# Kernel tuning notes

Measured on AMD Instinct MI355X. Metric: run time of the kernel, lower is better.

The kernel has to match this reference:

```python
import jax, jax.numpy as jnp
import numpy as np

D_MODEL = 768
N_LAYER = 2
VOCAB = 32000
D_STATE = 16
D_INNER = 1536
DT_RANK = 48
D_CONV = 4
B, L = 2, 1024
EPS = 1e-5


def rmsnorm(x, w):
    return x * jax.lax.rsqrt(jnp.mean(x * x, axis=-1, keepdims=True) + EPS) * w


def selective_scan(u, dt, A, Bm, Cm, Dv):
    # u: (b,l,d)  dt: (b,l,d)  A: (d,n)  Bm,Cm: (b,l,n)  Dv: (d,)
    dA = jnp.einsum('bld,dn->bldn', dt, A)
    dB_u = jnp.einsum('bld,bld,bln->bldn', dt, u, Bm)
    # shift dA left by one step along l, zero-pad at end, reverse-cumsum, exp
    t = jnp.concatenate([dA[:, 1:], jnp.zeros_like(dA[:, :1])], axis=1)
    dA_cumsum = jnp.exp(jnp.flip(jnp.cumsum(jnp.flip(t, axis=1), axis=1), axis=1))
    x = dB_u * dA_cumsum
    x = jnp.cumsum(x, axis=1) / (dA_cumsum + 1e-12)
    y = jnp.einsum('bldn,bln->bld', x, Cm)
    return y + u * Dv


def mamba_block(x, W_in, conv_w, conv_b, x_proj_w, dt_proj_w, dt_proj_b, A_log, D_param, W_out):
    b, l, d = x.shape
    xz = x @ W_in.T                       # (b,l,2*d_inner)
    xs, res = xz[..., :D_INNER], xz[..., D_INNER:]
    # depthwise causal conv1d: left-pad d_conv-1 -> output length l
    xt = jnp.transpose(xs, (0, 2, 1))     # (b,d_in,l)
    xt = jax.lax.conv_general_dilated(
        xt, conv_w, window_strides=(1,), padding=[(D_CONV - 1, 0)],
        dimension_numbers=('NCH', 'OIH', 'NCH'), feature_group_count=D_INNER)
    xt = xt + conv_b[None, :, None]
    xs = jax.nn.silu(jnp.transpose(xt, (0, 2, 1)))
    # SSM
    A = -jnp.exp(A_log.astype(jnp.float32))
    x_dbl = xs @ x_proj_w.T               # (b,l,dt_rank+2n)
    delta = x_dbl[..., :DT_RANK]
    Bm = x_dbl[..., DT_RANK:DT_RANK + D_STATE]
    Cm = x_dbl[..., DT_RANK + D_STATE:]
    delta = jax.nn.softplus(delta @ dt_proj_w.T + dt_proj_b)
    y = selective_scan(xs, delta, A, Bm, Cm, D_param.astype(jnp.float32))
    y = y * jax.nn.silu(res)
    return y @ W_out.T


def setup_inputs() -> dict:
    key = jax.random.key(0)
    ks = jax.random.split(key, 12)
    s = 0.02
    inp = {
        'input_ids': jax.random.randint(ks[0], (B, L), 0, VOCAB),
        'embedding': jax.random.normal(ks[1], (VOCAB, D_MODEL), jnp.float32) * s,
        'W_in': jax.random.normal(ks[2], (N_LAYER, 2 * D_INNER, D_MODEL), jnp.float32) * s,
        'conv_w': jax.random.normal(ks[3], (N_LAYER, D_INNER, 1, D_CONV), jnp.float32) * 0.2,
        'conv_b': jnp.zeros((N_LAYER, D_INNER), jnp.float32),
        'x_proj_w': jax.random.normal(ks[4], (N_LAYER, DT_RANK + 2 * D_STATE, D_INNER), jnp.float32) * s,
        'dt_proj_w': jax.random.normal(ks[5], (N_LAYER, D_INNER, DT_RANK), jnp.float32) * s,
        'dt_proj_b': jnp.full((N_LAYER, D_INNER), -4.0, jnp.float32),
        'A_log': jnp.broadcast_to(jnp.log(jnp.arange(1, D_STATE + 1, dtype=jnp.float32)), (N_LAYER, D_INNER, D_STATE)) * jnp.ones((N_LAYER, D_INNER, 1), jnp.float32),
        'D_param': jnp.ones((N_LAYER, D_INNER), jnp.float32),
        'W_out': jax.random.normal(ks[6], (N_LAYER, D_MODEL, D_INNER), jnp.float32) * s,
        'norm_w': jnp.ones((N_LAYER, D_MODEL), jnp.float32),
        'norm_f_w': jnp.ones((D_MODEL,), jnp.float32),
    }
    return inp


def reference(input_ids, embedding, W_in, conv_w, conv_b, x_proj_w, dt_proj_w,
              dt_proj_b, A_log, D_param, W_out, norm_w, norm_f_w):
    x = embedding[input_ids]              # (b,l,d_model)
    for i in range(N_LAYER):
        x = mamba_block(rmsnorm(x, norm_w[i]), W_in[i], conv_w[i], conv_b[i],
                        x_proj_w[i], dt_proj_w[i], dt_proj_b[i], A_log[i],
                        D_param[i], W_out[i]) + x
    x = rmsnorm(x, norm_f_w)
    return x @ embedding.T                # tied lm_head -> (b,l,vocab)
```

## Files before the change

### kernel.cpp

```cpp
#include <hip/hip_runtime.h>
#include <math.h>

#define DM    768
#define DS    16
#define DI    1536
#define DTR   48
#define NB    2
#define NL    1024
#define NBL   (NB*NL)
#define NVOC  32000
#define XDL   128

typedef __attribute__((ext_vector_type(8))) short bf16x8;
typedef __attribute__((ext_vector_type(4))) float floatx4;

static __device__ __forceinline__ float siluf(float x){ return x / (1.0f + expf(-x)); }
static __device__ __forceinline__ float softplusf(float x){ return (x > 20.0f) ? x : log1pf(expf(x)); }
static __device__ __forceinline__ unsigned short f2bf(float f){
    unsigned int u = __float_as_uint(f);
    u += 0x7FFFu + ((u >> 16) & 1u);
    return (unsigned short)(u >> 16);
}

#define GLL16(g, l) __builtin_amdgcn_global_load_lds( \
    (const __attribute__((address_space(1))) unsigned int*)(g), \
    (__attribute__((address_space(3))) unsigned int*)(l), 16, 0, 0)

__global__ __launch_bounds__(256) void cast_bf16_kernel(const float* __restrict__ in,
        unsigned short* __restrict__ out, int n4){
    int i = blockIdx.x*256 + threadIdx.x;
    if (i >= n4) return;
    float4 v = ((const float4*)in)[i];
    ushort4 o = { f2bf(v.x), f2bf(v.y), f2bf(v.z), f2bf(v.w) };
    ((ushort4*)out)[i] = o;
}

__global__ __launch_bounds__(256) void cast_pad_xproj_kernel(const float* __restrict__ in,
        unsigned short* __restrict__ out){
    int q = blockIdx.x*256 + threadIdx.x;
    const int QL = 128*1536/4;
    if (q >= 2*QL) return;
    int layer = q / QL, rem = q - layer*QL;
    int row = rem / (1536/4), c4 = rem - row*(1536/4);
    ushort4 o = {0,0,0,0};
    if (row < 80){
        float4 v = ((const float4*)(in + ((size_t)layer*80 + row)*1536))[c4];
        o.x = f2bf(v.x); o.y = f2bf(v.y); o.z = f2bf(v.z); o.w = f2bf(v.w);
    }
    ((ushort4*)out)[q] = o;
}

__global__ __launch_bounds__(256) void zero_f32_kernel(float* __restrict__ p, int n4){
    int i = blockIdx.x*256 + threadIdx.x;
    if (i >= n4) return;
    float4 z = {0.f,0.f,0.f,0.f};
    ((float4*)p)[i] = z;
}

__global__ __launch_bounds__(256) void embed_kernel(const int* __restrict__ ids,
        const float* __restrict__ emb, float* __restrict__ x){
    int i = blockIdx.x*256 + threadIdx.x;
    if (i >= NBL*DM) return;
    int row = i / DM, c = i - row*DM;
    x[i] = emb[(size_t)ids[row]*DM + c];
}

__global__ __launch_bounds__(256) void rmsnorm_bf16_kernel(const float* __restrict__ x,
        const float* __restrict__ w, unsigned short* __restrict__ h){
    int row = blockIdx.x;
    const float* xr = x + (size_t)row*DM;
    __shared__ float red[4];
    int tid = threadIdx.x, lane = tid & 63, wv = tid >> 6;
    float s = 0.f;
    for (int c = tid; c < DM; c += 256){ float v = xr[c]; s += v*v; }
    #pragma unroll
    for (int o = 32; o > 0; o >>= 1) s += __shfl_xor(s, o, 64);
    if (lane == 0) red[wv] = s;
    __syncthreads();
    float tot = red[0] + red[1] + red[2] + red[3];
    float r = 1.0f / sqrtf(tot*(1.0f/DM) + 1e-5f);
    for (int c = tid; c < DM; c += 256) h[(size_t)row*DM + c] = f2bf(xr[c]*r*w[c]);
}

template<int MODE>
__global__ __launch_bounds__(256) void mfma_gemm_nt(const unsigned short* __restrict__ A,
        const unsigned short* __restrict__ B, float* __restrict__ C,
        int M, int N, int K, int Kc){
    __shared__ __align__(16) unsigned short Asm[2][128*64];
    __shared__ __align__(16) unsigned short Bsm[2][128*64];
    int tid = threadIdx.x;

    int nwg  = gridDim.x * gridDim.y;
    int orig = blockIdx.y * gridDim.x + blockIdx.x;
    int q = nwg >> 3, r = nwg & 7;
    int xcd = orig & 7;
    int wg  = (xcd < r ? xcd*(q+1) : r*(q+1) + (xcd-r)*q) + (orig >> 3);
    int mb  = wg % gridDim.y;
    int nb  = wg / gridDim.y;
    int m0 = mb * 128, n0 = nb * 128;

    int lane = tid & 63;
    int quad = lane >> 4, l16 = lane & 15;
    int wave = tid >> 6;
    int wm = (wave >> 1) * 64, wn = (wave & 1) * 64;

    floatx4 acc[4][4] = {};

    int srow = tid >> 3;
    int csrc = ((tid & 7) ^ ((tid >> 3) & 7)) * 8;
    const unsigned short* Ag = A + (size_t)(m0 + srow) * K + csrc;
    const unsigned short* Bg = B + (size_t)(n0 + srow) * K + csrc;

    int k0 = blockIdx.z * Kc;
    int nsteps = Kc >> 6;

    #pragma unroll
    for (int qr = 0; qr < 4; qr++){
        GLL16(Ag + (size_t)qr*32*K + k0, &Asm[0][(qr*256 + tid)*8]);
        GLL16(Bg + (size_t)qr*32*K + k0, &Bsm[0][(qr*256 + tid)*8]);
    }
    __syncthreads();

    int cur = 0;
    for (int s = 0; s < nsteps; s++){
        if (s + 1 < nsteps){
            int kt = k0 + (s+1)*64;
            #pragma unroll
            for (int qr = 0; qr < 4; qr++){
                GLL16(Ag + (size_t)qr*32*K + kt, &Asm[cur^1][(qr*256 + tid)*8]);
                GLL16(Bg + (size_t)qr*32*K + kt, &Bsm[cur^1][(qr*256 + tid)*8]);
            }
        }

        #pragma unroll
        for (int ks = 0; ks < 2; ks++){
            bf16x8 af[4], bff[4];
            #pragma unroll
            for (int i = 0; i < 4; i++){
                int ar = wm + i*16 + l16;
                af[i]  = *(const bf16x8*)&Asm[cur][ar*64 + ((ks*4 + quad) ^ (ar & 7))*8];
                int br = wn + i*16 + l16;
                bff[i] = *(const bf16x8*)&Bsm[cur][br*64 + ((ks*4 + quad) ^ (br & 7))*8];
            }
            #pragma unroll
            for (int i = 0; i < 4; i++)
                #pragma unroll
                for (int j = 0; j < 4; j++)
                    acc[i][j] = __builtin_amdgcn_mfma_f32_16x16x32_bf16(af[i], bff[j], acc[i][j], 0, 0, 0);
        }
        __syncthreads();
        cur ^= 1;
    }

    #pragma unroll
    for (int i = 0; i < 4; i++){
        int gm = m0 + wm + i*16 + quad*4;
        #pragma unroll
        for (int j = 0; j < 4; j++){
            int gn = n0 + wn + j*16 + l16;
            float* cp = C + (size_t)gm*N + gn;
            #pragma unroll
            for (int rr = 0; rr < 4; rr++){
                float v = acc[i][j][rr];
                if (MODE == 2){
                    atomicAdd(&cp[(size_t)rr*N], v);
                } else {
                    if (MODE == 1) v += cp[(size_t)rr*N];
                    cp[(size_t)rr*N] = v;
                }
            }
        }
    }
}

__global__ __launch_bounds__(256) void gemm_nt(const float* __restrict__ A,
        const float* __restrict__ Bw, float* __restrict__ C, const float* __restrict__ bias,
        int M, int N, int K, int lda, int ldb, int ldc, int act, int accum){
    __shared__ float As[16][68];
    __shared__ float Bs[16][68];
    int tid = threadIdx.x;
    int tn = tid & 15, tm = tid >> 4;
    int n0 = blockIdx.x * 64, m0 = blockIdx.y * 64;
    float acc[4][4] = {{0.f}};
    for (int kt = 0; kt < K; kt += 16){
        int gk = kt + tn;
        bool kok = gk < K;
        #pragma unroll
        for (int r = 0; r < 4; r++){
            int m = tm + r*16;
            As[tn][m] = (kok && (m0 + m) < M) ? A[(size_t)(m0+m)*lda + gk] : 0.f;
            Bs[tn][m] = (kok && (n0 + m) < N) ? Bw[(size_t)(n0+m)*ldb + gk] : 0.f;
        }
        __syncthreads();
        #pragma unroll
        for (int kk = 0; kk < 16; kk++){
            float a0 = As[kk][tm*4+0], a1 = As[kk][tm*4+1], a2 = As[kk][tm*4+2], a3 = As[kk][tm*4+3];
            float b0 = Bs[kk][tn*4+0], b1 = Bs[kk][tn*4+1], b2 = Bs[kk][tn*4+2], b3 = Bs[kk][tn*4+3];
            acc[0][0] += a0*b0; acc[0][1] += a0*b1; acc[0][2] += a0*b2; acc[0][3] += a0*b3;
            acc[1][0] += a1*b0; acc[1][1] += a1*b1; acc[1][2] += a1*b2; acc[1][3] += a1*b3;
            acc[2][0] += a2*b0; acc[2][1] += a2*b1; acc[2][2] += a2*b2; acc[2][3] += a2*b3;
            acc[3][0] += a3*b0; acc[3][1] += a3*b1; acc[3][2] += a3*b2; acc[3][3] += a3*b3;
        }
        __syncthreads();
    }
    #pragma unroll
    for (int i = 0; i < 4; i++){
        int gm = m0 + tm*4 + i;
        if (gm >= M) continue;
        #pragma unroll
        for (int j = 0; j < 4; j++){
            int gn = n0 + tn*4 + j;
            if (gn >= N) continue;
            float v = acc[i][j];
            if (bias) v += bias[gn];
            if (act == 1) v = softplusf(v);
            size_t ci = (size_t)gm*ldc + gn;
            if (accum) v += C[ci];
            C[ci] = v;
        }
    }
}

__global__ __launch_bounds__(256) void conv_silu_kernel(const float* __restrict__ xz,
        const float* __restrict__ cw, const float* __restrict__ cb,
        float* __restrict__ xs, unsigned short* __restrict__ xs_bf){
    int i = blockIdx.x*256 + threadIdx.x;
    if (i >= NBL*DI) return;
    int bl = i / DI, d = i - bl*DI;
    int l = bl & (NL-1);
    float acc = cb[d];
    #pragma unroll
    for (int j = 0; j < 4; j++){
        int off = j - 3;
        if (l + off >= 0) acc += cw[d*4+j] * xz[(size_t)(bl + off)*(2*DI) + d];
    }
    float v = siluf(acc);
    xs[i] = v;
    xs_bf[i] = f2bf(v);
}

__global__ __launch_bounds__(256) void transpose_kernel(const float* __restrict__ in,
        float* __restrict__ out, int R, int Ccols, int ldin){
    __shared__ float tile[32][33];
    int c0 = blockIdx.x*32, r0 = blockIdx.y*32;
    int tx = threadIdx.x & 31, ty = threadIdx.x >> 5;
    #pragma unroll
    for (int i = 0; i < 32; i += 8){
        int r = r0 + ty + i, c = c0 + tx;
        tile[ty+i][tx] = (r < R && c < Ccols) ? in[(size_t)r*ldin + c] : 0.f;
    }
    __syncthreads();
    #pragma unroll
    for (int i = 0; i < 32; i += 8){
        int r = r0 + tx, c = c0 + ty + i;
        if (c < Ccols && r < R) out[(size_t)c*R + r] = tile[tx][ty+i];
    }
}

__global__ __launch_bounds__(256) void transpose2_kernel(const float* __restrict__ in1,
        float* __restrict__ out1, const float* __restrict__ in2, float* __restrict__ out2){
    __shared__ float tile[32][33];
    int c0 = blockIdx.x*32, r0 = blockIdx.y*32;
    int tx = threadIdx.x & 31, ty = threadIdx.x >> 5;
    #pragma unroll
    for (int i = 0; i < 32; i += 8)
        tile[ty+i][tx] = in1[(size_t)(r0+ty+i)*DI + (c0+tx)];
    __syncthreads();
    #pragma unroll
    for (int i = 0; i < 32; i += 8)
        out1[(size_t)(c0+ty+i)*NBL + (r0+tx)] = tile[tx][ty+i];
    __syncthreads();
    #pragma unroll
    for (int i = 0; i < 32; i += 8)
        tile[ty+i][tx] = in2[(size_t)(r0+ty+i)*DI + (c0+tx)];
    __syncthreads();
    #pragma unroll
    for (int i = 0; i < 32; i += 8)
        out2[(size_t)(c0+ty+i)*NBL + (r0+tx)] = tile[tx][ty+i];
}

static __device__ __forceinline__ float wave_incl_scan(float v, int lane){
    #pragma unroll
    for (int s = 1; s < 64; s <<= 1){
        float t = __shfl_up(v, s, 64);
        if (lane >= s) v += t;
    }
    return v;
}

__global__ __launch_bounds__(256) void scan_kernel(const float* __restrict__ u_t,
        const float* dt_t, const float* __restrict__ xdbl_t,
        const float* __restrict__ A_log, const float* __restrict__ Dp,
        float* y_t){
    int tid = threadIdx.x, lane = tid & 63, w = tid >> 6;
    int bd = blockIdx.x*4 + w;
    int b = bd / DI, d = bd - b*DI;
    size_t rowoff = (size_t)d*NBL + b*NL;
    int l0 = lane*16;

    float d16[16], u16[16];
    #pragma unroll
    for (int q = 0; q < 4; q++){
        float4 v = ((const float4*)(dt_t + rowoff + l0))[q];
        d16[q*4+0]=v.x; d16[q*4+1]=v.y; d16[q*4+2]=v.z; d16[q*4+3]=v.w;
        float4 u = ((const float4*)(u_t + rowoff + l0))[q];
        u16[q*4+0]=u.x; u16[q*4+1]=u.y; u16[q*4+2]=u.z; u16[q*4+3]=u.w;
    }
    float pl[16], yac[16];
    float run = 0.f;
    #pragma unroll
    for (int r = 0; r < 16; r++){ run += d16[r]; pl[r] = run; yac[r] = 0.f; }
    float inc = wave_incl_scan(run, lane);
    float ex  = inc - run;
    float T   = __shfl(inc, 63, 64);
    #pragma unroll
    for (int r = 0; r < 16; r++) pl[r] += ex;

    for (int n = 0; n < DS; n++){
        float An = -expf(A_log[d*DS + n]);
        float Bv[16], Cv[16];
        #pragma unroll
        for (int q = 0; q < 4; q++){
            float4 bv = ((const float4*)(xdbl_t + (size_t)(DTR+n)*NBL + b*NL + l0))[q];
            Bv[q*4+0]=bv.x; Bv[q*4+1]=bv.y; Bv[q*4+2]=bv.z; Bv[q*4+3]=bv.w;
            float4 cv = ((const float4*)(xdbl_t + (size_t)(DTR+DS+n)*NBL + b*NL + l0))[q];
            Cv[q*4+0]=cv.x; Cv[q*4+1]=cv.y; Cv[q*4+2]=cv.z; Cv[q*4+3]=cv.w;
        }
        float e[16], zl[16];
        float zrun = 0.f;
        #pragma unroll
        for (int r = 0; r < 16; r++){
            e[r] = expf(An * (T - pl[r]));
            zrun += d16[r]*u16[r]*Bv[r]*e[r];
            zl[r] = zrun;
        }
        float zinc = wave_incl_scan(zrun, lane);
        float zex  = zinc - zrun;
        #pragma unroll
        for (int r = 0; r < 16; r++){
            float num = zex + zl[r];
            yac[r] += num / (e[r] + 1e-12f) * Cv[r];
        }
    }
    float Dv = Dp[d];
    #pragma unroll
    for (int q = 0; q < 4; q++){
        float4 yo;
        yo.x = yac[q*4+0] + u16[q*4+0]*Dv;
        yo.y = yac[q*4+1] + u16[q*4+1]*Dv;
        yo.z = yac[q*4+2] + u16[q*4+2]*Dv;
        yo.w = yac[q*4+3] + u16[q*4+3]*Dv;
        ((float4*)(y_t + rowoff + l0))[q] = yo;
    }
}

__global__ __launch_bounds__(256) void gate_transpose_kernel(const float* __restrict__ y_t,
        const float* __restrict__ xz, unsigned short* __restrict__ ys){
    __shared__ float tile[32][33];
    int c0 = blockIdx.x*32;
    int r0 = blockIdx.y*32;
    int tx = threadIdx.x & 31, ty = threadIdx.x >> 5;
    #pragma unroll
    for (int i = 0; i < 32; i += 8)
        tile[ty+i][tx] = y_t[(size_t)(r0+ty+i)*NBL + (c0+tx)];
    __syncthreads();
    #pragma unroll
    for (int i = 0; i < 32; i += 8){
        int d  = r0 + tx;
        int bl = c0 + ty + i;
        float g = siluf(xz[(size_t)bl*(2*DI) + DI + d]);
        ys[(size_t)bl*DI + d] = f2bf(tile[tx][ty+i] * g);
    }
}

extern "C" void kernel_launch(void* const* d_in, const int* in_sizes, int n_in,
                              void* d_out, int out_size, void* d_ws, size_t ws_size,
                              hipStream_t stream){
    const int*   ids    = (const int*)d_in[0];
    const float* emb    = (const float*)d_in[1];
    const float* W_in   = (const float*)d_in[2];
    const float* convw  = (const float*)d_in[3];
    const float* convb  = (const float*)d_in[4];
    const float* xproj  = (const float*)d_in[5];
    const float* dtw    = (const float*)d_in[6];
    const float* dtbias = (const float*)d_in[7];
    const float* Alog   = (const float*)d_in[8];
    const float* Dpar   = (const float*)d_in[9];
    const float* Wout   = (const float*)d_in[10];
    const float* normw  = (const float*)d_in[11];
    const float* normf  = (const float*)d_in[12];
    float* out = (float*)d_out;

    float* ws    = (float*)d_ws;
    float* x     = ws;
    float* xz    = x     + (size_t)NBL*DM;
    float* xs    = xz    + (size_t)NBL*2*DI;
    float* xdbl  = xs    + (size_t)NBL*DI;
    float* xdblt = xdbl  + (size_t)NBL*XDL;
    float* dtb   = xdblt + (size_t)NBL*80;
    float* dtt   = dtb   + (size_t)NBL*DI;
    float* ut    = dtt   + (size_t)NBL*DI;
    unsigned short* h_bf   = (unsigned short*)(ut + (size_t)NBL*DI);
    unsigned short* emb_bf = h_bf    + (size_t)NBL*DM;
    unsigned short* win_bf = emb_bf  + (size_t)NVOC*DM;
    unsigned short* wout_bf= win_bf  + (size_t)2*2*DI*DM;
    unsigned short* xs_bf  = wout_bf + (size_t)2*DM*DI;
    unsigned short* xprojp = xs_bf   + (size_t)NBL*DI;
    unsigned short* ys_bf  = (unsigned short*)dtb;
    float* yt = dtt;

    cast_bf16_kernel<<<(NVOC*DM/4 + 255)/256, 256, 0, stream>>>(emb, emb_bf, NVOC*DM/4);
    cast_bf16_kernel<<<(2*2*DI*DM/4 + 255)/256, 256, 0, stream>>>(W_in, win_bf, 2*2*DI*DM/4);
    cast_bf16_kernel<<<(2*DM*DI/4 + 255)/256, 256, 0, stream>>>(Wout, wout_bf, 2*DM*DI/4);
    cast_pad_xproj_kernel<<<(2*128*1536/4 + 255)/256, 256, 0, stream>>>(xproj, xprojp);

    embed_kernel<<<(NBL*DM + 255)/256, 256, 0, stream>>>(ids, emb, x);

    for (int i = 0; i < 2; i++){
        rmsnorm_bf16_kernel<<<NBL, 256, 0, stream>>>(x, normw + i*DM, h_bf);
        mfma_gemm_nt<0><<<dim3(3072/128, NBL/128, 1), 256, 0, stream>>>(
                h_bf, win_bf + (size_t)i*2*DI*DM, xz, NBL, 2*DI, DM, DM);
        conv_silu_kernel<<<(NBL*DI + 255)/256, 256, 0, stream>>>(xz, convw + i*DI*4, convb + i*DI, xs, xs_bf);
        zero_f32_kernel<<<(NBL*XDL/4 + 255)/256, 256, 0, stream>>>(xdbl, NBL*XDL/4);
        mfma_gemm_nt<2><<<dim3(1, NBL/128, 8), 256, 0, stream>>>(
                xs_bf, xprojp + (size_t)i*128*DI, xdbl, NBL, XDL, DI, DI/8);
        gemm_nt<<<dim3(24,32), 256, 0, stream>>>(xdbl, dtw + (size_t)i*DI*DTR, dtb, dtbias + i*DI,
                NBL, DI, DTR, XDL, DTR, DI, 1, 0);
        transpose_kernel<<<dim3(3,64),  256, 0, stream>>>(xdbl, xdblt, NBL, 80, XDL);
        transpose2_kernel<<<dim3(48,64), 256, 0, stream>>>(dtb, dtt, xs, ut);
        scan_kernel<<<NB*DI/4, 256, 0, stream>>>(ut, dtt, xdblt,
                Alog + (size_t)i*DI*DS, Dpar + i*DI, yt);
        gate_transpose_kernel<<<dim3(64,48), 256, 0, stream>>>(yt, xz, ys_bf);
        mfma_gemm_nt<2><<<dim3(DM/128, NBL/128, 2), 256, 0, stream>>>(
                ys_bf, wout_bf + (size_t)i*DM*DI, x, NBL, DM, DI, DI/2);
    }

    rmsnorm_bf16_kernel<<<NBL, 256, 0, stream>>>(x, normf, h_bf);
    mfma_gemm_nt<0><<<dim3(NVOC/128, NBL/128, 1), 256, 0, stream>>>(
            h_bf, emb_bf, out, NBL, NVOC, DM, DM);
}
```

Baseline: 877.6 us.

## Triple-buffer MFMA GEMM with BK=32 and move dt_proj onto MFMA with fused softplus

The shared bf16 MFMA GEMM moves from a double-buffered K-step of 64 to a triple-buffered K-step of 32. It uses explicit vmcnt waits and a single barrier per step, so global-to-LDS loads run two stages ahead of compute. Separately, the scalar fp32 dt_proj GEMM is replaced by the MFMA GEMM with a new epilogue mode that adds the bias and applies softplus. That path needs an extra cast of x_dbl to bf16 and a zero-padded bf16 copy of dt_proj_w, and it adds bf16 rounding to delta.

```diff
diff --git a/kernel.cpp b/kernel.cpp
--- a/kernel.cpp
+++ b/kernel.cpp
@@ -50,6 +50,19 @@
     ((ushort4*)out)[q] = o;
 }
 
+__global__ __launch_bounds__(256) void cast_pad_dtw_kernel(const float* __restrict__ in,
+        unsigned short* __restrict__ out){
+    int q = blockIdx.x*256 + threadIdx.x;
+    if (q >= 2*1536*32) return;
+    int row = q >> 5, qc = q & 31;
+    ushort4 o = {0,0,0,0};
+    if (qc < 12){
+        float4 v = *(const float4*)(in + (size_t)row*48 + qc*4);
+        o.x = f2bf(v.x); o.y = f2bf(v.y); o.z = f2bf(v.z); o.w = f2bf(v.w);
+    }
+    ((ushort4*)out)[q] = o;
+}
+
 __global__ __launch_bounds__(256) void zero_f32_kernel(float* __restrict__ p, int n4){
     int i = blockIdx.x*256 + threadIdx.x;
     if (i >= n4) return;
@@ -85,9 +98,9 @@
 template<int MODE>
 __global__ __launch_bounds__(256) void mfma_gemm_nt(const unsigned short* __restrict__ A,
         const unsigned short* __restrict__ B, float* __restrict__ C,
-        int M, int N, int K, int Kc){
-    __shared__ __align__(16) unsigned short Asm[2][128*64];
-    __shared__ __align__(16) unsigned short Bsm[2][128*64];
+        const float* __restrict__ bias, int M, int N, int K, int Kc){
+    __shared__ __align__(16) unsigned short Asm[3][128*32];
+    __shared__ __align__(16) unsigned short Bsm[3][128*32];
     int tid = threadIdx.x;
 
     int nwg  = gridDim.x * gridDim.y;
@@ -106,51 +119,60 @@
 
     floatx4 acc[4][4] = {};
 
-    int srow = tid >> 3;
-    int csrc = ((tid & 7) ^ ((tid >> 3) & 7)) * 8;
+    int srow = tid >> 2;
+    int csrc = ((tid & 3) ^ ((tid >> 2) & 3) ^ ((tid >> 4) & 3)) * 8;
     const unsigned short* Ag = A + (size_t)(m0 + srow) * K + csrc;
     const unsigned short* Bg = B + (size_t)(n0 + srow) * K + csrc;
+    size_t half = (size_t)64 * K;
 
     int k0 = blockIdx.z * Kc;
-    int nsteps = Kc >> 6;
-
-    #pragma unroll
-    for (int qr = 0; qr < 4; qr++){
-        GLL16(Ag + (size_t)qr*32*K + k0, &Asm[0][(qr*256 + tid)*8]);
-        GLL16(Bg + (size_t)qr*32*K + k0, &Bsm[0][(qr*256 + tid)*8]);
-    }
-    __syncthreads();
+    int nsteps = Kc >> 5;
+
+#define STAGE(buf, step) do{ int kk_ = k0 + (step)*32;                      \
+        GLL16(Ag + kk_,        &Asm[buf][(size_t)tid*8]);                   \
+        GLL16(Ag + kk_ + half, &Asm[buf][2048 + (size_t)tid*8]);            \
+        GLL16(Bg + kk_,        &Bsm[buf][(size_t)tid*8]);                   \
+        GLL16(Bg + kk_ + half, &Bsm[buf][2048 + (size_t)tid*8]); }while(0)
+#define WAITV4 asm volatile("s_waitcnt vmcnt(4)" ::: "memory")
+#define WAITV0 asm volatile("s_waitcnt vmcnt(0)" ::: "memory")
+
+    STAGE(0, 0);
+    if (nsteps > 1) STAGE(1, 1);
+    if (nsteps > 1) { WAITV4; } else { WAITV0; }
+    __builtin_amdgcn_s_barrier();
+    __builtin_amdgcn_sched_barrier(0);
 
     int cur = 0;
     for (int s = 0; s < nsteps; s++){
+        if (s + 2 < nsteps){
+            int b2 = cur + 2; if (b2 >= 3) b2 -= 3;
+            STAGE(b2, s + 2);
+        }
+
+        bf16x8 af[4], bff[4];
+        #pragma unroll
+        for (int i = 0; i < 4; i++){
+            int ar = wm + i*16 + l16;
+            af[i]  = *(const bf16x8*)&Asm[cur][ar*32 + ((quad ^ (ar & 3) ^ ((ar >> 2) & 3)))*8];
+            int br = wn + i*16 + l16;
+            bff[i] = *(const bf16x8*)&Bsm[cur][br*32 + ((quad ^ (br & 3) ^ ((br >> 2) & 3)))*8];
+        }
+        #pragma unroll
+        for (int i = 0; i < 4; i++)
+            #pragma unroll
+            for (int j = 0; j < 4; j++)
+                acc[i][j] = __builtin_amdgcn_mfma_f32_16x16x32_bf16(af[i], bff[j], acc[i][j], 0, 0, 0);
+
         if (s + 1 < nsteps){
-            int kt = k0 + (s+1)*64;
-            #pragma unroll
-            for (int qr = 0; qr < 4; qr++){
-                GLL16(Ag + (size_t)qr*32*K + kt, &Asm[cur^1][(qr*256 + tid)*8]);
-                GLL16(Bg + (size_t)qr*32*K + kt, &Bsm[cur^1][(qr*256 + tid)*8]);
-            }
-        }
-
-        #pragma unroll
-        for (int ks = 0; ks < 2; ks++){
-            bf16x8 af[4], bff[4];
-            #pragma unroll
-            for (int i = 0; i < 4; i++){
-                int ar = wm + i*16 + l16;
-                af[i]  = *(const bf16x8*)&Asm[cur][ar*64 + ((ks*4 + quad) ^ (ar & 7))*8];
-                int br = wn + i*16 + l16;
-                bff[i] = *(const bf16x8*)&Bsm[cur][br*64 + ((ks*4 + quad) ^ (br & 7))*8];
-            }
-            #pragma unroll
-            for (int i = 0; i < 4; i++)
-                #pragma unroll
-                for (int j = 0; j < 4; j++)
-                    acc[i][j] = __builtin_amdgcn_mfma_f32_16x16x32_bf16(af[i], bff[j], acc[i][j], 0, 0, 0);
-        }
-        __syncthreads();
-        cur ^= 1;
-    }
+            if (s + 2 < nsteps) { WAITV4; } else { WAITV0; }
+            __builtin_amdgcn_s_barrier();
+            __builtin_amdgcn_sched_barrier(0);
+            cur = (cur + 1 == 3) ? 0 : cur + 1;
+        }
+    }
+#undef STAGE
+#undef WAITV4
+#undef WAITV0
 
     #pragma unroll
     for (int i = 0; i < 4; i++){
@@ -164,59 +186,13 @@
                 float v = acc[i][j][rr];
                 if (MODE == 2){
                     atomicAdd(&cp[(size_t)rr*N], v);
+                } else if (MODE == 3){
+                    cp[(size_t)rr*N] = softplusf(v + bias[gn]);
                 } else {
                     if (MODE == 1) v += cp[(size_t)rr*N];
                     cp[(size_t)rr*N] = v;
                 }
             }
-        }
-    }
-}
-
-__global__ __launch_bounds__(256) void gemm_nt(const float* __restrict__ A,
-        const float* __restrict__ Bw, float* __restrict__ C, const float* __restrict__ bias,
-        int M, int N, int K, int lda, int ldb, int ldc, int act, int accum){
-    __shared__ float As[16][68];
-    __shared__ float Bs[16][68];
-    int tid = threadIdx.x;
-    int tn = tid & 15, tm = tid >> 4;
-    int n0 = blockIdx.x * 64, m0 = blockIdx.y * 64;
-    float acc[4][4] = {{0.f}};
-    for (int kt = 0; kt < K; kt += 16){
-        int gk = kt + tn;
-        bool kok = gk < K;
-        #pragma unroll
-        for (int r = 0; r < 4; r++){
-            int m = tm + r*16;
-            As[tn][m] = (kok && (m0 + m) < M) ? A[(size_t)(m0+m)*lda + gk] : 0.f;
-            Bs[tn][m] = (kok && (n0 + m) < N) ? Bw[(size_t)(n0+m)*ldb + gk] : 0.f;
-        }
-        __syncthreads();
-        #pragma unroll
-        for (int kk = 0; kk < 16; kk++){
-            float a0 = As[kk][tm*4+0], a1 = As[kk][tm*4+1], a2 = As[kk][tm*4+2], a3 = As[kk][tm*4+3];
-            float b0 = Bs[kk][tn*4+0], b1 = Bs[kk][tn*4+1], b2 = Bs[kk][tn*4+2], b3 = Bs[kk][tn*4+3];
-            acc[0][0] += a0*b0; acc[0][1] += a0*b1; acc[0][2] += a0*b2; acc[0][3] += a0*b3;
-            acc[1][0] += a1*b0; acc[1][1] += a1*b1; acc[1][2] += a1*b2; acc[1][3] += a1*b3;
-            acc[2][0] += a2*b0; acc[2][1] += a2*b1; acc[2][2] += a2*b2; acc[2][3] += a2*b3;
-            acc[3][0] += a3*b0; acc[3][1] += a3*b1; acc[3][2] += a3*b2; acc[3][3] += a3*b3;
-        }
-        __syncthreads();
-    }
-    #pragma unroll
-    for (int i = 0; i < 4; i++){
-        int gm = m0 + tm*4 + i;
-        if (gm >= M) continue;
-        #pragma unroll
-        for (int j = 0; j < 4; j++){
-            int gn = n0 + tn*4 + j;
-            if (gn >= N) continue;
-            float v = acc[i][j];
-            if (bias) v += bias[gn];
-            if (act == 1) v = softplusf(v);
-            size_t ci = (size_t)gm*ldc + gn;
-            if (accum) v += C[ci];
-            C[ci] = v;
         }
     }
 }
@@ -406,6 +382,8 @@
     unsigned short* wout_bf= win_bf  + (size_t)2*2*DI*DM;
     unsigned short* xs_bf  = wout_bf + (size_t)2*DM*DI;
     unsigned short* xprojp = xs_bf   + (size_t)NBL*DI;
+    unsigned short* xdbl_bf= xprojp  + (size_t)2*128*DI;
+    unsigned short* dtw_bf = xdbl_bf + (size_t)NBL*XDL;
     unsigned short* ys_bf  = (unsigned short*)dtb;
     float* yt = dtt;
 
@@ -413,29 +391,31 @@
     cast_bf16_kernel<<<(2*2*DI*DM/4 + 255)/256, 256, 0, stream>>>(W_in, win_bf, 2*2*DI*DM/4);
     cast_bf16_kernel<<<(2*DM*DI/4 + 255)/256, 256, 0, stream>>>(Wout, wout_bf, 2*DM*DI/4);
     cast_pad_xproj_kernel<<<(2*128*1536/4 + 255)/256, 256, 0, stream>>>(xproj, xprojp);
+    cast_pad_dtw_kernel<<<(2*1536*32 + 255)/256, 256, 0, stream>>>(dtw, dtw_bf);
 
     embed_kernel<<<(NBL*DM + 255)/256, 256, 0, stream>>>(ids, emb, x);
 
     for (int i = 0; i < 2; i++){
         rmsnorm_bf16_kernel<<<NBL, 256, 0, stream>>>(x, normw + i*DM, h_bf);
         mfma_gemm_nt<0><<<dim3(3072/128, NBL/128, 1), 256, 0, stream>>>(
-                h_bf, win_bf + (size_t)i*2*DI*DM, xz, NBL, 2*DI, DM, DM);
+                h_bf, win_bf + (size_t)i*2*DI*DM, xz, nullptr, NBL, 2*DI, DM, DM);
         conv_silu_kernel<<<(NBL*DI + 255)/256, 256, 0, stream>>>(xz, convw + i*DI*4, convb + i*DI, xs, xs_bf);
         zero_f32_kernel<<<(NBL*XDL/4 + 255)/256, 256, 0, stream>>>(xdbl, NBL*XDL/4);
         mfma_gemm_nt<2><<<dim3(1, NBL/128, 8), 256, 0, stream>>>(
-                xs_bf, xprojp + (size_t)i*128*DI, xdbl, NBL, XDL, DI, DI/8);
-        gemm_nt<<<dim3(24,32), 256, 0, stream>>>(xdbl, dtw + (size_t)i*DI*DTR, dtb, dtbias + i*DI,
-                NBL, DI, DTR, XDL, DTR, DI, 1, 0);
+                xs_bf, xprojp + (size_t)i*128*DI, xdbl, nullptr, NBL, XDL, DI, DI/8);
+        cast_bf16_kernel<<<(NBL*XDL/4 + 255)/256, 256, 0, stream>>>(xdbl, xdbl_bf, NBL*XDL/4);
+        mfma_gemm_nt<3><<<dim3(DI/128, NBL/128, 1), 256, 0, stream>>>(
+                xdbl_bf, dtw_bf + (size_t)i*DI*XDL, dtb, dtbias + i*DI, NBL, DI, XDL, XDL);
         transpose_kernel<<<dim3(3,64),  256, 0, stream>>>(xdbl, xdblt, NBL, 80, XDL);
         transpose2_kernel<<<dim3(48,64), 256, 0, stream>>>(dtb, dtt, xs, ut);
         scan_kernel<<<NB*DI/4, 256, 0, stream>>>(ut, dtt, xdblt,
                 Alog + (size_t)i*DI*DS, Dpar + i*DI, yt);
         gate_transpose_kernel<<<dim3(64,48), 256, 0, stream>>>(yt, xz, ys_bf);
         mfma_gemm_nt<2><<<dim3(DM/128, NBL/128, 2), 256, 0, stream>>>(
-                ys_bf, wout_bf + (size_t)i*DM*DI, x, NBL, DM, DI, DI/2);
+                ys_bf, wout_bf + (size_t)i*DM*DI, x, nullptr, NBL, DM, DI, DI/2);
     }
 
     rmsnorm_bf16_kernel<<<NBL, 256, 0, stream>>>(x, normf, h_bf);
     mfma_gemm_nt<0><<<dim3(NVOC/128, NBL/128, 1), 256, 0, stream>>>(
-            h_bf, emb_bf, out, NBL, NVOC, DM, DM);
-}
+            h_bf, emb_bf, out, nullptr, NBL, NVOC, DM, DM);
+}
```

Result: no change. 886.7 us (+1.0%).

## Add 256x256 ping-pong GEMM for LM head and triple-buffer generic MFMA GEMM

Applied to the files above, without the earlier changes.

Adds a new 512-thread GEMM with 256x256 tiles for the vocab projection. It interleaves global-to-LDS loads with MFMA phases using explicit vmcnt waits, barriers and priority hints, so memory traffic overlaps with compute. The existing 128x128 GEMM moves to K=32 steps with a three-stage LDS buffer, a new swizzle, and waitcnt-based synchronisation in place of __syncthreads. An unused bias parameter is added. The risk lies in the hand-tuned waitcnt counts, which must match the load order exactly, and in higher register and LDS pressure.

```diff
diff --git a/kernel.cpp b/kernel.cpp
--- a/kernel.cpp
+++ b/kernel.cpp
@@ -25,6 +25,9 @@
 #define GLL16(g, l) __builtin_amdgcn_global_load_lds( \
     (const __attribute__((address_space(1))) unsigned int*)(g), \
     (__attribute__((address_space(3))) unsigned int*)(l), 16, 0, 0)
+
+#define WAITVM(n) do{ asm volatile("s_waitcnt vmcnt(" #n ")" ::: "memory"); \
+                      __builtin_amdgcn_sched_barrier(0); }while(0)
 
 __global__ __launch_bounds__(256) void cast_bf16_kernel(const float* __restrict__ in,
         unsigned short* __restrict__ out, int n4){
@@ -82,12 +85,158 @@
     for (int c = tid; c < DM; c += 256) h[(size_t)row*DM + c] = f2bf(xr[c]*r*w[c]);
 }
 
+__global__ __launch_bounds__(512, 2) void gemm256(const unsigned short* __restrict__ A,
+        const unsigned short* __restrict__ B, float* __restrict__ C,
+        int M, int N, int K){
+    __shared__ __align__(16) unsigned short Asm[2][2][128*64];
+    __shared__ __align__(16) unsigned short Bsm[2][2][128*64];
+    int tid = threadIdx.x;
+
+    int nwg  = gridDim.x * gridDim.y;
+    int orig = blockIdx.y * gridDim.x + blockIdx.x;
+    int qq = nwg >> 3, r8 = nwg & 7;
+    int xcd = orig & 7;
+    int wg  = (xcd < r8 ? xcd*(qq+1) : r8*(qq+1) + (xcd-r8)*qq) + (orig >> 3);
+    int mb  = wg % gridDim.y;
+    int nb  = wg / gridDim.y;
+    int m0 = mb*256, n0 = nb*256;
+
+    int lane = tid & 63, wave = tid >> 6;
+    int wr = wave >> 2, wc = wave & 3;
+    int quad = lane >> 4, l16 = lane & 15;
+
+    int srow = tid >> 3;
+    int csrc = ((tid & 7) ^ ((tid >> 3) & 7)) * 8;
+    const unsigned short* Ag = A + (size_t)(m0 + srow)*K + csrc;
+    const unsigned short* Bg = B + (size_t)(n0 + srow)*K + csrc;
+    int NT = K >> 6;
+
+    floatx4 acc[8][4] = {};
+
+#define ST_A(tt, h) do{ \
+    GLL16(Ag + (size_t)((h)*128)*K      + (size_t)(tt)*64, &Asm[(tt)&1][h][(size_t)tid*8]); \
+    GLL16(Ag + (size_t)((h)*128 + 64)*K + (size_t)(tt)*64, &Asm[(tt)&1][h][4096 + (size_t)tid*8]); \
+}while(0)
+#define ST_B(tt, h) do{ \
+    GLL16(Bg + (size_t)((h)*128)*K      + (size_t)(tt)*64, &Bsm[(tt)&1][h][(size_t)tid*8]); \
+    GLL16(Bg + (size_t)((h)*128 + 64)*K + (size_t)(tt)*64, &Bsm[(tt)&1][h][4096 + (size_t)tid*8]); \
+}while(0)
+#define LDA_(tt, h, jj, ks) (*(const bf16x8*)&Asm[(tt)&1][h][((jj)*32 + wr*16 + l16)*64 + ((((ks)*4 + quad) ^ (l16 & 7))*8)])
+#define LDB_(tt, k, ks)     (*(const bf16x8*)&Bsm[(tt)&1][wc>>1][((wc&1)*64 + (k)*16 + l16)*64 + ((((ks)*4 + quad) ^ (l16 & 7))*8)])
+#define MM(d, x, y) d = __builtin_amdgcn_mfma_f32_16x16x32_bf16(x, y, d, 0, 0, 0)
+
+    ST_A(0, 0); ST_B(0, 0); ST_B(0, 1); ST_A(0, 1);
+    if (NT > 1){ ST_A(1, 0); ST_B(1, 0); ST_B(1, 1); WAITVM(8); }
+    else       { WAITVM(0); }
+    __builtin_amdgcn_s_barrier();
+
+    for (int t = 0; t < NT; ++t){
+        bf16x8 a[8], b0[4], b1[4];
+        #pragma unroll
+        for (int jj = 0; jj < 4; jj++){
+            a[jj*2+0] = LDA_(t, 0, jj, 0);
+            a[jj*2+1] = LDA_(t, 0, jj, 1);
+        }
+        #pragma unroll
+        for (int k = 0; k < 2; k++){
+            b0[k*2+0] = LDB_(t, k, 0);
+            b0[k*2+1] = LDB_(t, k, 1);
+        }
+        if (t + 1 < NT) ST_A(t+1, 1);
+        __builtin_amdgcn_s_barrier();
+        __builtin_amdgcn_s_setprio(1);
+        #pragma unroll
+        for (int jj = 0; jj < 4; jj++)
+            #pragma unroll
+            for (int fn = 0; fn < 2; fn++){
+                MM(acc[jj][fn], a[jj*2+0], b0[fn*2+0]);
+                MM(acc[jj][fn], a[jj*2+1], b0[fn*2+1]);
+            }
+        __builtin_amdgcn_s_setprio(0);
+        __builtin_amdgcn_s_barrier();
+
+        #pragma unroll
+        for (int k = 0; k < 2; k++){
+            b1[k*2+0] = LDB_(t, k+2, 0);
+            b1[k*2+1] = LDB_(t, k+2, 1);
+        }
+        if (t + 2 < NT) ST_A(t+2, 0);
+        __builtin_amdgcn_s_barrier();
+        __builtin_amdgcn_s_setprio(1);
+        #pragma unroll
+        for (int jj = 0; jj < 4; jj++)
+            #pragma unroll
+            for (int fn = 0; fn < 2; fn++){
+                MM(acc[jj][fn+2], a[jj*2+0], b1[fn*2+0]);
+                MM(acc[jj][fn+2], a[jj*2+1], b1[fn*2+1]);
+            }
+        __builtin_amdgcn_s_setprio(0);
+        if (t == NT-1)      { WAITVM(0); }
+        else if (t == NT-2) { WAITVM(8); }
+        else                { WAITVM(10); }
+        __builtin_amdgcn_s_barrier();
+
+        #pragma unroll
+        for (int jj = 0; jj < 4; jj++){
+            a[jj*2+0] = LDA_(t, 1, jj, 0);
+            a[jj*2+1] = LDA_(t, 1, jj, 1);
+        }
+        if (t + 2 < NT) ST_B(t+2, 0);
+        __builtin_amdgcn_s_barrier();
+        __builtin_amdgcn_s_setprio(1);
+        #pragma unroll
+        for (int jj = 0; jj < 4; jj++)
+            #pragma unroll
+            for (int fn = 0; fn < 2; fn++){
+                MM(acc[4+jj][fn], a[jj*2+0], b0[fn*2+0]);
+                MM(acc[4+jj][fn], a[jj*2+1], b0[fn*2+1]);
+            }
+        __builtin_amdgcn_s_setprio(0);
+        __builtin_amdgcn_s_barrier();
+
+        if (t + 2 < NT) ST_B(t+2, 1);
+        __builtin_amdgcn_s_barrier();
+        __builtin_amdgcn_s_setprio(1);
+        #pragma unroll
+        for (int jj = 0; jj < 4; jj++)
+            #pragma unroll
+            for (int fn = 0; fn < 2; fn++){
+                MM(acc[4+jj][fn+2], a[jj*2+0], b1[fn*2+0]);
+                MM(acc[4+jj][fn+2], a[jj*2+1], b1[fn*2+1]);
+            }
+        __builtin_amdgcn_s_setprio(0);
+        if (t + 1 < NT){
+            if (t == NT-2) { WAITVM(2); }
+            else           { WAITVM(8); }
+        }
+        __builtin_amdgcn_s_barrier();
+    }
+#undef ST_A
+#undef ST_B
+#undef LDA_
+#undef LDB_
+#undef MM
+
+    #pragma unroll
+    for (int j = 0; j < 8; j++){
+        int gm = m0 + j*32 + wr*16 + quad*4;
+        #pragma unroll
+        for (int fn = 0; fn < 4; fn++){
+            int gn = n0 + wc*64 + fn*16 + l16;
+            float* cp = C + (size_t)gm*N + gn;
+            #pragma unroll
+            for (int rr = 0; rr < 4; rr++)
+                cp[(size_t)rr*N] = acc[j][fn][rr];
+        }
+    }
+}
+
 template<int MODE>
 __global__ __launch_bounds__(256) void mfma_gemm_nt(const unsigned short* __restrict__ A,
         const unsigned short* __restrict__ B, float* __restrict__ C,
-        int M, int N, int K, int Kc){
-    __shared__ __align__(16) unsigned short Asm[2][128*64];
-    __shared__ __align__(16) unsigned short Bsm[2][128*64];
+        const float* __restrict__ bias, int M, int N, int K, int Kc){
+    __shared__ __align__(16) unsigned short Asm[3][128*32];
+    __shared__ __align__(16) unsigned short Bsm[3][128*32];
     int tid = threadIdx.x;
 
     int nwg  = gridDim.x * gridDim.y;
@@ -106,51 +255,54 @@
 
     floatx4 acc[4][4] = {};
 
-    int srow = tid >> 3;
-    int csrc = ((tid & 7) ^ ((tid >> 3) & 7)) * 8;
+    int srow = tid >> 2;
+    int csrc = ((tid & 3) ^ ((tid >> 2) & 3) ^ ((tid >> 4) & 3)) * 8;
     const unsigned short* Ag = A + (size_t)(m0 + srow) * K + csrc;
     const unsigned short* Bg = B + (size_t)(n0 + srow) * K + csrc;
+    size_t half = (size_t)64 * K;
 
     int k0 = blockIdx.z * Kc;
-    int nsteps = Kc >> 6;
-
-    #pragma unroll
-    for (int qr = 0; qr < 4; qr++){
-        GLL16(Ag + (size_t)qr*32*K + k0, &Asm[0][(qr*256 + tid)*8]);
-        GLL16(Bg + (size_t)qr*32*K + k0, &Bsm[0][(qr*256 + tid)*8]);
-    }
-    __syncthreads();
+    int nsteps = Kc >> 5;
+
+#define STAGE(buf, step) do{ int kk_ = k0 + (step)*32;                      \
+        GLL16(Ag + kk_,        &Asm[buf][(size_t)tid*8]);                   \
+        GLL16(Ag + kk_ + half, &Asm[buf][2048 + (size_t)tid*8]);            \
+        GLL16(Bg + kk_,        &Bsm[buf][(size_t)tid*8]);                   \
+        GLL16(Bg + kk_ + half, &Bsm[buf][2048 + (size_t)tid*8]); }while(0)
+
+    STAGE(0, 0);
+    if (nsteps > 1) STAGE(1, 1);
+    if (nsteps > 1) { WAITVM(4); } else { WAITVM(0); }
+    __builtin_amdgcn_s_barrier();
 
     int cur = 0;
     for (int s = 0; s < nsteps; s++){
+        if (s + 2 < nsteps){
+            int b2 = cur + 2; if (b2 >= 3) b2 -= 3;
+            STAGE(b2, s + 2);
+        }
+
+        bf16x8 af[4], bff[4];
+        #pragma unroll
+        for (int i = 0; i < 4; i++){
+            int ar = wm + i*16 + l16;
+            af[i]  = *(const bf16x8*)&Asm[cur][ar*32 + ((quad ^ (ar & 3) ^ ((ar >> 2) & 3)))*8];
+            int br = wn + i*16 + l16;
+            bff[i] = *(const bf16x8*)&Bsm[cur][br*32 + ((quad ^ (br & 3) ^ ((br >> 2) & 3)))*8];
+        }
+        #pragma unroll
+        for (int i = 0; i < 4; i++)
+            #pragma unroll
+            for (int j = 0; j < 4; j++)
+                acc[i][j] = __builtin_amdgcn_mfma_f32_16x16x32_bf16(af[i], bff[j], acc[i][j], 0, 0, 0);
+
         if (s + 1 < nsteps){
-            int kt = k0 + (s+1)*64;
-            #pragma unroll
-            for (int qr = 0; qr < 4; qr++){
-                GLL16(Ag + (size_t)qr*32*K + kt, &Asm[cur^1][(qr*256 + tid)*8]);
-                GLL16(Bg + (size_t)qr*32*K + kt, &Bsm[cur^1][(qr*256 + tid)*8]);
-            }
-        }
-
-        #pragma unroll
-        for (int ks = 0; ks < 2; ks++){
-            bf16x8 af[4], bff[4];
-            #pragma unroll
-            for (int i = 0; i < 4; i++){
-                int ar = wm + i*16 + l16;
-                af[i]  = *(const bf16x8*)&Asm[cur][ar*64 + ((ks*4 + quad) ^ (ar & 7))*8];
-                int br = wn + i*16 + l16;
-                bff[i] = *(const bf16x8*)&Bsm[cur][br*64 + ((ks*4 + quad) ^ (br & 7))*8];
-            }
-            #pragma unroll
-            for (int i = 0; i < 4; i++)
-                #pragma unroll
-                for (int j = 0; j < 4; j++)
-                    acc[i][j] = __builtin_amdgcn_mfma_f32_16x16x32_bf16(af[i], bff[j], acc[i][j], 0, 0, 0);
-        }
-        __syncthreads();
-        cur ^= 1;
-    }
+            if (s + 2 < nsteps) { WAITVM(4); } else { WAITVM(0); }
+            __builtin_amdgcn_s_barrier();
+            cur = (cur + 1 == 3) ? 0 : cur + 1;
+        }
+    }
+#undef STAGE
 
     #pragma unroll
     for (int i = 0; i < 4; i++){
@@ -419,11 +571,11 @@
     for (int i = 0; i < 2; i++){
         rmsnorm_bf16_kernel<<<NBL, 256, 0, stream>>>(x, normw + i*DM, h_bf);
         mfma_gemm_nt<0><<<dim3(3072/128, NBL/128, 1), 256, 0, stream>>>(
-                h_bf, win_bf + (size_t)i*2*DI*DM, xz, NBL, 2*DI, DM, DM);
+                h_bf, win_bf + (size_t)i*2*DI*DM, xz, nullptr, NBL, 2*DI, DM, DM);
         conv_silu_kernel<<<(NBL*DI + 255)/256, 256, 0, stream>>>(xz, convw + i*DI*4, convb + i*DI, xs, xs_bf);
         zero_f32_kernel<<<(NBL*XDL/4 + 255)/256, 256, 0, stream>>>(xdbl, NBL*XDL/4);
         mfma_gemm_nt<2><<<dim3(1, NBL/128, 8), 256, 0, stream>>>(
-                xs_bf, xprojp + (size_t)i*128*DI, xdbl, NBL, XDL, DI, DI/8);
+                xs_bf, xprojp + (size_t)i*128*DI, xdbl, nullptr, NBL, XDL, DI, DI/8);
         gemm_nt<<<dim3(24,32), 256, 0, stream>>>(xdbl, dtw + (size_t)i*DI*DTR, dtb, dtbias + i*DI,
                 NBL, DI, DTR, XDL, DTR, DI, 1, 0);
         transpose_kernel<<<dim3(3,64),  256, 0, stream>>>(xdbl, xdblt, NBL, 80, XDL);
@@ -432,10 +584,10 @@
                 Alog + (size_t)i*DI*DS, Dpar + i*DI, yt);
         gate_transpose_kernel<<<dim3(64,48), 256, 0, stream>>>(yt, xz, ys_bf);
         mfma_gemm_nt<2><<<dim3(DM/128, NBL/128, 2), 256, 0, stream>>>(
-                ys_bf, wout_bf + (size_t)i*DM*DI, x, NBL, DM, DI, DI/2);
+                ys_bf, wout_bf + (size_t)i*DM*DI, x, nullptr, NBL, DM, DI, DI/2);
     }
 
     rmsnorm_bf16_kernel<<<NBL, 256, 0, stream>>>(x, normf, h_bf);
-    mfma_gemm_nt<0><<<dim3(NVOC/128, NBL/128, 1), 256, 0, stream>>>(
-            h_bf, emb_bf, out, NBL, NVOC, DM, DM);
-}
+    gemm256<<<dim3(NVOC/256, NBL/256), 512, 0, stream>>>(
+            h_bf, emb_bf, out, NBL, NVOC, DM);
+}
```

Measured after the change: 843.1 us. 3.9% less time.
